# Optimization experiments

Measured on AMD Instinct MI355X. Metric: run time of the kernel, lower is better.

Reference implementation:

```python
import jax, jax.numpy as jnp
import numpy as np

B = 524288
LATENT = 64
LEVELS = (8.0, 8.0, 8.0, 2.0)
FSQ = 4
NUM_CODES = 1024  # prod(levels)
STRIDES = (1, 8, 64, 512)  # mixed-radix strides, strides[i] = prod(levels[:i])


def _orthogonal(key, shape):
    # mimic nn.init.orthogonal_ for a (rows, cols) weight
    rows, cols = shape
    n = max(rows, cols)
    a = jax.random.normal(key, (n, n), jnp.float32)
    q, r = jnp.linalg.qr(a)
    q = q * jnp.sign(jnp.diag(r))[None, :]
    return q[:rows, :cols]


def setup_inputs() -> dict:
    key = jax.random.key(0)
    k1, k2, k3 = jax.random.split(key, 3)
    z_e = jax.random.normal(k1, (B, LATENT), jnp.float32)
    W_in = _orthogonal(k2, (FSQ, LATENT))    # proj_in.weight
    W_out = _orthogonal(k3, (LATENT, FSQ))   # proj_out.weight
    return {"z_e": z_e, "W_in": W_in, "W_out": W_out}


def reference(z_e, W_in, W_out):
    levels = jnp.asarray(LEVELS, jnp.float32)          # (fsq_dim,)
    strides = jnp.asarray(STRIDES, jnp.int32)          # (fsq_dim,)

    # proj_in: (B, latent) @ (latent, fsq) -> (B, fsq)
    z_fsq = z_e @ W_in.T

    # FSQ quantization with straight-through estimator
    z_unit = (jnp.tanh(z_fsq) + 1.0) * 0.5
    z_scaled = z_unit * (levels - 1.0)
    z_q_nonneg = z_scaled + jax.lax.stop_gradient(jnp.round(z_scaled) - z_scaled)
    z_q_nonneg = jnp.clip(z_q_nonneg, 0.0, levels - 1.0)
    z_q_centered = z_q_nonneg - (levels - 1.0) * 0.5

    # proj_out: (B, fsq) @ (fsq, latent) -> (B, latent)
    z_q_latent = z_q_centered @ W_out.T
    z_q = z_e + jax.lax.stop_gradient(z_q_latent - z_e)

    # indices via mixed-radix encoding (int, no grad)
    z_int = jnp.round(jax.lax.stop_gradient(z_q_nonneg)).astype(jnp.int32)
    z_int = jnp.clip(z_int, 0, (levels - 1.0).astype(jnp.int32))
    indices = jnp.sum(z_int * strides, axis=-1)        # (B,)

    # histogram-based perplexity/utilization (fused scatter-add, no B x num_codes one-hot)
    counts = jnp.zeros((NUM_CODES,), jnp.float32).at[indices].add(1.0)
    avg_probs = counts / jnp.float32(z_e.shape[0])
    perplexity = jnp.exp(-jnp.sum(avg_probs * jnp.log(avg_probs + 1e-10)))
    utilization = jnp.mean((avg_probs > 0).astype(jnp.float32))

    commitment_loss = jnp.float32(0.0)
    codebook_loss = jnp.float32(0.0)
    return z_q, indices, commitment_loss, codebook_loss, perplexity, utilization
```

## Files before the change

### kernel.cpp

```cpp
#include <hip/hip_runtime.h>
#include <math.h>

#define NROWS 524288
#define LATENT 64
#define NUM_CODES 1024
#define BLOCK 256
#define GRID 1024
#define ROWS_PER_BLOCK (NROWS / GRID)
#define LANES_PER_ROW 8
#define ROWS_PER_ITER (BLOCK / LANES_PER_ROW)
#define NITER (ROWS_PER_BLOCK / ROWS_PER_ITER)

typedef float v4f __attribute__((ext_vector_type(4)));

__device__ __forceinline__ v4f ldnt4(const float* p) {
    return __builtin_nontemporal_load((const v4f*)p);
}
__device__ __forceinline__ void stnt4(float* p, v4f v) {
    __builtin_nontemporal_store(v, (v4f*)p);
}

__device__ __forceinline__ float dot8(v4f a, v4f wa, v4f b, v4f wb) {
    float r = a.x * wa.x;
    r = fmaf(a.y, wa.y, r); r = fmaf(a.z, wa.z, r); r = fmaf(a.w, wa.w, r);
    r = fmaf(b.x, wb.x, r); r = fmaf(b.y, wb.y, r);
    r = fmaf(b.z, wb.z, r); r = fmaf(b.w, wb.w, r);
    return r;
}

__device__ __forceinline__ float q7(float s, int& bin) {
    float t  = tanhf(s);
    float zs = (t + 1.0f) * 0.5f * 7.0f;
    float r  = rintf(zs);
    r = fminf(fmaxf(r, 0.0f), 7.0f);
    bin = (int)r;
    return r - 3.5f;
}

__global__ __launch_bounds__(BLOCK) void fsq_main(
    const float* __restrict__ z_e,
    const float* __restrict__ W_in,
    const float* __restrict__ W_out,
    float* __restrict__ z_q,
    float* __restrict__ idx_out,
    unsigned int* __restrict__ counts,
    unsigned int* __restrict__ hists,
    int atomic_flush)
{
    __shared__ unsigned int lhist[NUM_CODES];
    const int tid = threadIdx.x;
    for (int i = tid; i < NUM_CODES; i += BLOCK) lhist[i] = 0;
    if (!atomic_flush && blockIdx.x == 0) {
        for (int i = tid; i < NUM_CODES; i += BLOCK) counts[i] = 0;
    }

    const int sub = tid & (LANES_PER_ROW - 1);
    const int rid = tid >> 3;
    const int l0  = sub * 4;

    v4f winA[4], winB[4], woA[4], woB[4];
    #pragma unroll
    for (int f = 0; f < 4; ++f) {
        winA[f] = *(const v4f*)(W_in + f * LATENT + l0);
        winB[f] = *(const v4f*)(W_in + f * LATENT + 32 + l0);
    }
    #pragma unroll
    for (int j = 0; j < 4; ++j) {
        woA[j] = *(const v4f*)(W_out + (l0 + j) * 4);
        woB[j] = *(const v4f*)(W_out + (32 + l0 + j) * 4);
    }

    __syncthreads();

    const size_t row0 = (size_t)blockIdx.x * ROWS_PER_BLOCK + rid;
    const float* p = z_e + row0 * LATENT + l0;

    v4f vA = ldnt4(p);
    v4f vB = ldnt4(p + 32);

    for (int it = 0; it < NITER; ++it) {
        v4f nA, nB;
        if (it + 1 < NITER) {
            const float* pn = p + (size_t)(it + 1) * ROWS_PER_ITER * LATENT;
            nA = ldnt4(pn);
            nB = ldnt4(pn + 32);
        }

        float s0 = dot8(vA, winA[0], vB, winB[0]);
        float s1 = dot8(vA, winA[1], vB, winB[1]);
        float s2 = dot8(vA, winA[2], vB, winB[2]);
        float s3 = dot8(vA, winA[3], vB, winB[3]);

        #pragma unroll
        for (int m = 1; m < LANES_PER_ROW; m <<= 1) {
            s0 += __shfl_xor(s0, m);
            s1 += __shfl_xor(s1, m);
            s2 += __shfl_xor(s2, m);
            s3 += __shfl_xor(s3, m);
        }

        int b0, b1, b2;
        const float c0 = q7(s0, b0);
        const float c1 = q7(s1, b1);
        const float c2 = q7(s2, b2);
        const int   b3 = (s3 > 0.0f) ? 1 : 0;
        const float c3 = (float)b3 - 0.5f;

        v4f oA, oB;
        oA.x = fmaf(c0, woA[0].x, fmaf(c1, woA[0].y, fmaf(c2, woA[0].z, c3 * woA[0].w)));
        oA.y = fmaf(c0, woA[1].x, fmaf(c1, woA[1].y, fmaf(c2, woA[1].z, c3 * woA[1].w)));
        oA.z = fmaf(c0, woA[2].x, fmaf(c1, woA[2].y, fmaf(c2, woA[2].z, c3 * woA[2].w)));
        oA.w = fmaf(c0, woA[3].x, fmaf(c1, woA[3].y, fmaf(c2, woA[3].z, c3 * woA[3].w)));
        oB.x = fmaf(c0, woB[0].x, fmaf(c1, woB[0].y, fmaf(c2, woB[0].z, c3 * woB[0].w)));
        oB.y = fmaf(c0, woB[1].x, fmaf(c1, woB[1].y, fmaf(c2, woB[1].z, c3 * woB[1].w)));
        oB.z = fmaf(c0, woB[2].x, fmaf(c1, woB[2].y, fmaf(c2, woB[2].z, c3 * woB[2].w)));
        oB.w = fmaf(c0, woB[3].x, fmaf(c1, woB[3].y, fmaf(c2, woB[3].z, c3 * woB[3].w)));

        const size_t row = row0 + (size_t)it * ROWS_PER_ITER;
        float* q = z_q + row * LATENT + l0;
        stnt4(q, oA);
        stnt4(q + 32, oB);

        if (sub == 0) {
            const int idx = b0 + (b1 << 3) + (b2 << 6) + (b3 << 9);
            atomicAdd(&lhist[idx], 1u);
            __builtin_nontemporal_store((float)idx, idx_out + row);
        }

        vA = nA;
        vB = nB;
    }

    __syncthreads();

    if (atomic_flush) {
        for (int i = tid; i < NUM_CODES; i += BLOCK) {
            const unsigned int c = lhist[i];
            if (c) atomicAdd(&counts[i], c);
        }
    } else {
        unsigned int* dst = hists + (size_t)blockIdx.x * NUM_CODES;
        for (int i = tid; i < NUM_CODES; i += BLOCK) dst[i] = lhist[i];
    }
}

#define RED_BLOCKS 128
#define HISTS_PER_RED (GRID / RED_BLOCKS)

__global__ __launch_bounds__(256) void reduce_hist(
    const unsigned int* __restrict__ hists,
    unsigned int* __restrict__ counts)
{
    const int t = threadIdx.x;
    unsigned int a0 = 0, a1 = 0, a2 = 0, a3 = 0;
    const int k0 = blockIdx.x * HISTS_PER_RED;
    for (int k = k0; k < k0 + HISTS_PER_RED; ++k) {
        const unsigned int* h = hists + (size_t)k * NUM_CODES;
        a0 += h[t];
        a1 += h[t + 256];
        a2 += h[t + 512];
        a3 += h[t + 768];
    }
    atomicAdd(&counts[t], a0);
    atomicAdd(&counts[t + 256], a1);
    atomicAdd(&counts[t + 512], a2);
    atomicAdd(&counts[t + 768], a3);
}

__global__ __launch_bounds__(1024) void fsq_stats(
    const unsigned int* __restrict__ counts,
    float* __restrict__ out_scalars)
{
    const int tid = threadIdx.x;
    const unsigned int c = counts[tid];

    const float p = (float)c / (float)NROWS;
    double t = (double)(p * logf(p + 1e-10f));
    int nz = (c != 0) ? 1 : 0;

    #pragma unroll
    for (int off = 32; off > 0; off >>= 1) {
        t  += __shfl_down(t, off);
        nz += __shfl_down(nz, off);
    }
    __shared__ double sh_t[16];
    __shared__ int    sh_nz[16];
    const int wid = tid >> 6;
    if ((tid & 63) == 0) { sh_t[wid] = t; sh_nz[wid] = nz; }
    __syncthreads();
    if (tid == 0) {
        double T = 0.0; int N = 0;
        #pragma unroll
        for (int i = 0; i < 16; ++i) { T += sh_t[i]; N += sh_nz[i]; }
        out_scalars[0] = 0.0f;
        out_scalars[1] = 0.0f;
        out_scalars[2] = expf((float)(-T));
        out_scalars[3] = (float)N / (float)NUM_CODES;
    }
}

extern "C" void kernel_launch(void* const* d_in, const int* in_sizes, int n_in,
                              void* d_out, int out_size, void* d_ws, size_t ws_size,
                              hipStream_t stream) {
    const float* z_e   = (const float*)d_in[0];
    const float* W_in  = (const float*)d_in[1];
    const float* W_out = (const float*)d_in[2];

    float* out     = (float*)d_out;
    float* zq      = out;
    float* idxs    = out + (size_t)NROWS * LATENT;
    float* scalars = idxs + NROWS;

    unsigned int* counts = (unsigned int*)d_ws;
    unsigned int* hists  = counts + NUM_CODES;

    const size_t need = (size_t)(GRID + 1) * NUM_CODES * sizeof(unsigned int);
    if (ws_size >= need) {
        fsq_main<<<GRID, BLOCK, 0, stream>>>(z_e, W_in, W_out, zq, idxs,
                                             counts, hists, 0);
        reduce_hist<<<RED_BLOCKS, 256, 0, stream>>>(hists, counts);
    } else {
        hipMemsetAsync(d_ws, 0, NUM_CODES * sizeof(unsigned int), stream);
        fsq_main<<<GRID, BLOCK, 0, stream>>>(z_e, W_in, W_out, zq, idxs,
                                             counts, hists, 1);
    }
    fsq_stats<<<1, 1024, 0, stream>>>(counts, scalars);
}
```

Baseline: 243.3 us.

## Process two rows per thread per iteration and flush histograms with global atomics

Each thread now handles two rows per loop iteration, 32 rows apart, with double-buffered prefetch of both. This raises memory-level parallelism and instruction-level parallelism. The per-block histogram dump and the separate reduce_hist kernel are replaced by a memset plus direct global atomicAdd of each nonzero bin. The kernel also gets launch_bounds with a min-blocks hint of 4, and the idx store is no longer nontemporal. The trade-off is more register pressure and atomic contention on the counts array in exchange for one fewer kernel launch and less workspace traffic.

```diff
diff --git a/kernel.cpp b/kernel.cpp
--- a/kernel.cpp
+++ b/kernel.cpp
@@ -8,7 +8,7 @@
 #define GRID 1024
 #define ROWS_PER_BLOCK (NROWS / GRID)
 #define LANES_PER_ROW 8
-#define ROWS_PER_ITER (BLOCK / LANES_PER_ROW)
+#define ROWS_PER_ITER 64
 #define NITER (ROWS_PER_BLOCK / ROWS_PER_ITER)
 
 typedef float v4f __attribute__((ext_vector_type(4)));
@@ -37,22 +37,57 @@
     return r - 3.5f;
 }
 
-__global__ __launch_bounds__(BLOCK) void fsq_main(
+struct RowRes { v4f oA, oB; int idx; };
+
+__device__ __forceinline__ RowRes process_row(
+    v4f vA, v4f vB,
+    const v4f winA[4], const v4f winB[4],
+    const v4f woA[4], const v4f woB[4])
+{
+    float s0 = dot8(vA, winA[0], vB, winB[0]);
+    float s1 = dot8(vA, winA[1], vB, winB[1]);
+    float s2 = dot8(vA, winA[2], vB, winB[2]);
+    float s3 = dot8(vA, winA[3], vB, winB[3]);
+
+    #pragma unroll
+    for (int m = 1; m < LANES_PER_ROW; m <<= 1) {
+        s0 += __shfl_xor(s0, m);
+        s1 += __shfl_xor(s1, m);
+        s2 += __shfl_xor(s2, m);
+        s3 += __shfl_xor(s3, m);
+    }
+
+    int b0, b1, b2;
+    const float c0 = q7(s0, b0);
+    const float c1 = q7(s1, b1);
+    const float c2 = q7(s2, b2);
+    const int   b3 = (s3 > 0.0f) ? 1 : 0;
+    const float c3 = (float)b3 - 0.5f;
+
+    RowRes r;
+    r.oA.x = fmaf(c0, woA[0].x, fmaf(c1, woA[0].y, fmaf(c2, woA[0].z, c3 * woA[0].w)));
+    r.oA.y = fmaf(c0, woA[1].x, fmaf(c1, woA[1].y, fmaf(c2, woA[1].z, c3 * woA[1].w)));
+    r.oA.z = fmaf(c0, woA[2].x, fmaf(c1, woA[2].y, fmaf(c2, woA[2].z, c3 * woA[2].w)));
+    r.oA.w = fmaf(c0, woA[3].x, fmaf(c1, woA[3].y, fmaf(c2, woA[3].z, c3 * woA[3].w)));
+    r.oB.x = fmaf(c0, woB[0].x, fmaf(c1, woB[0].y, fmaf(c2, woB[0].z, c3 * woB[0].w)));
+    r.oB.y = fmaf(c0, woB[1].x, fmaf(c1, woB[1].y, fmaf(c2, woB[1].z, c3 * woB[1].w)));
+    r.oB.z = fmaf(c0, woB[2].x, fmaf(c1, woB[2].y, fmaf(c2, woB[2].z, c3 * woB[2].w)));
+    r.oB.w = fmaf(c0, woB[3].x, fmaf(c1, woB[3].y, fmaf(c2, woB[3].z, c3 * woB[3].w)));
+    r.idx = b0 + (b1 << 3) + (b2 << 6) + (b3 << 9);
+    return r;
+}
+
+__global__ __launch_bounds__(BLOCK, 4) void fsq_main(
     const float* __restrict__ z_e,
     const float* __restrict__ W_in,
     const float* __restrict__ W_out,
     float* __restrict__ z_q,
     float* __restrict__ idx_out,
-    unsigned int* __restrict__ counts,
-    unsigned int* __restrict__ hists,
-    int atomic_flush)
+    unsigned int* __restrict__ counts)
 {
     __shared__ unsigned int lhist[NUM_CODES];
     const int tid = threadIdx.x;
     for (int i = tid; i < NUM_CODES; i += BLOCK) lhist[i] = 0;
-    if (!atomic_flush && blockIdx.x == 0) {
-        for (int i = tid; i < NUM_CODES; i += BLOCK) counts[i] = 0;
-    }
 
     const int sub = tid & (LANES_PER_ROW - 1);
     const int rid = tid >> 3;
@@ -72,99 +107,49 @@
 
     __syncthreads();
 
-    const size_t row0 = (size_t)blockIdx.x * ROWS_PER_BLOCK + rid;
-    const float* p = z_e + row0 * LATENT + l0;
-
-    v4f vA = ldnt4(p);
-    v4f vB = ldnt4(p + 32);
+    const size_t rowA0 = (size_t)blockIdx.x * ROWS_PER_BLOCK + rid;
+    const float* pA = z_e + rowA0 * LATENT + l0;
+    const float* pB = pA + 32 * LATENT;
+
+    v4f aA = ldnt4(pA), aB = ldnt4(pA + 32);
+    v4f bA = ldnt4(pB), bB = ldnt4(pB + 32);
 
     for (int it = 0; it < NITER; ++it) {
-        v4f nA, nB;
-        if (it + 1 < NITER) {
-            const float* pn = p + (size_t)(it + 1) * ROWS_PER_ITER * LATENT;
-            nA = ldnt4(pn);
-            nB = ldnt4(pn + 32);
+        v4f naA, naB, nbA, nbB;
+        const bool more = (it + 1 < NITER);
+        if (more) {
+            const float* qA = pA + (size_t)(it + 1) * ROWS_PER_ITER * LATENT;
+            const float* qB = qA + 32 * LATENT;
+            naA = ldnt4(qA); naB = ldnt4(qA + 32);
+            nbA = ldnt4(qB); nbB = ldnt4(qB + 32);
         }
 
-        float s0 = dot8(vA, winA[0], vB, winB[0]);
-        float s1 = dot8(vA, winA[1], vB, winB[1]);
-        float s2 = dot8(vA, winA[2], vB, winB[2]);
-        float s3 = dot8(vA, winA[3], vB, winB[3]);
-
-        #pragma unroll
-        for (int m = 1; m < LANES_PER_ROW; m <<= 1) {
-            s0 += __shfl_xor(s0, m);
-            s1 += __shfl_xor(s1, m);
-            s2 += __shfl_xor(s2, m);
-            s3 += __shfl_xor(s3, m);
+        const RowRes rA = process_row(aA, aB, winA, winB, woA, woB);
+        const RowRes rB = process_row(bA, bB, winA, winB, woA, woB);
+
+        const size_t rowA = rowA0 + (size_t)it * ROWS_PER_ITER;
+        const size_t rowB = rowA + 32;
+        float* qa = z_q + rowA * LATENT + l0;
+        float* qb = z_q + rowB * LATENT + l0;
+        stnt4(qa, rA.oA);       stnt4(qa + 32, rA.oB);
+        stnt4(qb, rB.oA);       stnt4(qb + 32, rB.oB);
+
+        if (sub == 0) {
+            atomicAdd(&lhist[rA.idx], 1u);
+            atomicAdd(&lhist[rB.idx], 1u);
+            idx_out[rowA] = (float)rA.idx;
+            idx_out[rowB] = (float)rB.idx;
         }
 
-        int b0, b1, b2;
-        const float c0 = q7(s0, b0);
-        const float c1 = q7(s1, b1);
-        const float c2 = q7(s2, b2);
-        const int   b3 = (s3 > 0.0f) ? 1 : 0;
-        const float c3 = (float)b3 - 0.5f;
-
-        v4f oA, oB;
-        oA.x = fmaf(c0, woA[0].x, fmaf(c1, woA[0].y, fmaf(c2, woA[0].z, c3 * woA[0].w)));
-        oA.y = fmaf(c0, woA[1].x, fmaf(c1, woA[1].y, fmaf(c2, woA[1].z, c3 * woA[1].w)));
-        oA.z = fmaf(c0, woA[2].x, fmaf(c1, woA[2].y, fmaf(c2, woA[2].z, c3 * woA[2].w)));
-        oA.w = fmaf(c0, woA[3].x, fmaf(c1, woA[3].y, fmaf(c2, woA[3].z, c3 * woA[3].w)));
-        oB.x = fmaf(c0, woB[0].x, fmaf(c1, woB[0].y, fmaf(c2, woB[0].z, c3 * woB[0].w)));
-        oB.y = fmaf(c0, woB[1].x, fmaf(c1, woB[1].y, fmaf(c2, woB[1].z, c3 * woB[1].w)));
-        oB.z = fmaf(c0, woB[2].x, fmaf(c1, woB[2].y, fmaf(c2, woB[2].z, c3 * woB[2].w)));
-        oB.w = fmaf(c0, woB[3].x, fmaf(c1, woB[3].y, fmaf(c2, woB[3].z, c3 * woB[3].w)));
-
-        const size_t row = row0 + (size_t)it * ROWS_PER_ITER;
-        float* q = z_q + row * LATENT + l0;
-        stnt4(q, oA);
-        stnt4(q + 32, oB);
-
-        if (sub == 0) {
-            const int idx = b0 + (b1 << 3) + (b2 << 6) + (b3 << 9);
-            atomicAdd(&lhist[idx], 1u);
-            __builtin_nontemporal_store((float)idx, idx_out + row);
-        }
-
-        vA = nA;
-        vB = nB;
+        if (more) { aA = naA; aB = naB; bA = nbA; bB = nbB; }
     }
 
     __syncthreads();
 
-    if (atomic_flush) {
-        for (int i = tid; i < NUM_CODES; i += BLOCK) {
-            const unsigned int c = lhist[i];
-            if (c) atomicAdd(&counts[i], c);
-        }
-    } else {
-        unsigned int* dst = hists + (size_t)blockIdx.x * NUM_CODES;
-        for (int i = tid; i < NUM_CODES; i += BLOCK) dst[i] = lhist[i];
-    }
-}
-
-#define RED_BLOCKS 128
-#define HISTS_PER_RED (GRID / RED_BLOCKS)
-
-__global__ __launch_bounds__(256) void reduce_hist(
-    const unsigned int* __restrict__ hists,
-    unsigned int* __restrict__ counts)
-{
-    const int t = threadIdx.x;
-    unsigned int a0 = 0, a1 = 0, a2 = 0, a3 = 0;
-    const int k0 = blockIdx.x * HISTS_PER_RED;
-    for (int k = k0; k < k0 + HISTS_PER_RED; ++k) {
-        const unsigned int* h = hists + (size_t)k * NUM_CODES;
-        a0 += h[t];
-        a1 += h[t + 256];
-        a2 += h[t + 512];
-        a3 += h[t + 768];
-    }
-    atomicAdd(&counts[t], a0);
-    atomicAdd(&counts[t + 256], a1);
-    atomicAdd(&counts[t + 512], a2);
-    atomicAdd(&counts[t + 768], a3);
+    for (int i = tid; i < NUM_CODES; i += BLOCK) {
+        const unsigned int c = lhist[i];
+        if (c) atomicAdd(&counts[i], c);
+    }
 }
 
 __global__ __launch_bounds__(1024) void fsq_stats(
@@ -212,17 +197,8 @@
     float* scalars = idxs + NROWS;
 
     unsigned int* counts = (unsigned int*)d_ws;
-    unsigned int* hists  = counts + NUM_CODES;
-
-    const size_t need = (size_t)(GRID + 1) * NUM_CODES * sizeof(unsigned int);
-    if (ws_size >= need) {
-        fsq_main<<<GRID, BLOCK, 0, stream>>>(z_e, W_in, W_out, zq, idxs,
-                                             counts, hists, 0);
-        reduce_hist<<<RED_BLOCKS, 256, 0, stream>>>(hists, counts);
-    } else {
-        hipMemsetAsync(d_ws, 0, NUM_CODES * sizeof(unsigned int), stream);
-        fsq_main<<<GRID, BLOCK, 0, stream>>>(z_e, W_in, W_out, zq, idxs,
-                                             counts, hists, 1);
-    }
+
+    hipMemsetAsync(counts, 0, NUM_CODES * sizeof(unsigned int), stream);
+    fsq_main<<<GRID, BLOCK, 0, stream>>>(z_e, W_in, W_out, zq, idxs, counts);
     fsq_stats<<<1, 1024, 0, stream>>>(counts, scalars);
 }
```

Result: no change. 241.6 us (-0.7%).
